# Performance work log

Hardware: AMD Instinct MI355X
Metric: run time of the kernel (lower is better)

The kernel has to match this reference:

```python
import jax, jax.numpy as jnp
import numpy as np

N = 50000
E = 800000
IN_C, HID, OUT_C = 512, 256, 128


def gcn_conv(x, edge_index, W, b, num_nodes):
    # PyG GCNConv: add self-loops, symmetric normalization, linear-then-aggregate.
    h = x @ W  # [N, out]
    src = jnp.concatenate([edge_index[0], jnp.arange(num_nodes)])
    dst = jnp.concatenate([edge_index[1], jnp.arange(num_nodes)])
    ones = jnp.ones(src.shape[0], dtype=x.dtype)
    deg = jax.ops.segment_sum(ones, dst, num_segments=num_nodes)  # in-degree incl. self-loop
    dinv = jax.lax.rsqrt(deg)  # deg >= 1 thanks to self-loops
    norm = dinv[src] * dinv[dst]  # [E+N]
    msg = h[src] * norm[:, None]  # gather + scale
    out = jax.ops.segment_sum(msg, dst, num_segments=num_nodes)  # scatter-add
    return out + b


def setup_inputs() -> dict:
    key = jax.random.key(0)
    k_x, k_e, k_w1, k_b1, k_w2, k_b2 = jax.random.split(key, 6)
    x = jax.random.normal(k_x, (N, IN_C), dtype=jnp.float32)
    edge_index = jax.random.randint(k_e, (2, E), 0, N, dtype=jnp.int64)
    s1 = 1.0 / np.sqrt(IN_C)
    s2 = 1.0 / np.sqrt(HID)
    W1 = jax.random.uniform(k_w1, (IN_C, HID), jnp.float32, -s1, s1)
    b1 = jax.random.uniform(k_b1, (HID,), jnp.float32, -s1, s1)
    W2 = jax.random.uniform(k_w2, (HID, OUT_C), jnp.float32, -s2, s2)
    b2 = jax.random.uniform(k_b2, (OUT_C,), jnp.float32, -s2, s2)
    return {"x": x, "edge_index": edge_index, "W1": W1, "b1": b1, "W2": W2, "b2": b2}


def reference(x, edge_index, W1, b1, W2, b2):
    h = gcn_conv(x, edge_index, W1, b1, N)
    h = jax.nn.relu(h)
    # dropout in eval mode == identity
    return gcn_conv(h, edge_index, W2, b2, N)
```

## Files before the change

### kernel.cpp

```cpp
#include <hip/hip_runtime.h>
#include <stdint.h>

typedef __bf16 bf16_t;
typedef bf16_t bf16x8 __attribute__((ext_vector_type(8)));
typedef bf16_t bf16x4 __attribute__((ext_vector_type(4)));
typedef bf16_t bf16x2 __attribute__((ext_vector_type(2)));
typedef float  f32x4  __attribute__((ext_vector_type(4)));

typedef __attribute__((address_space(3))) void* as3p;
typedef const __attribute__((address_space(1))) void* as1p;

#define IN_C 512
#define HID  256
#define OUTC 128

__global__ void k_prep(const float* __restrict__ W1, const float* __restrict__ W2,
                       const void* __restrict__ ei, int* __restrict__ flag,
                       int* __restrict__ cnt, bf16_t* __restrict__ W1t,
                       bf16_t* __restrict__ W2t, int n) {
  int t = blockIdx.x * blockDim.x + threadIdx.x;
  if (t < IN_C * HID) {
    W1t[(size_t)(t & 255) * IN_C + (t >> 8)] = (bf16_t)W1[t];
    return;
  }
  int u = t - IN_C * HID;
  if (u < HID * OUTC) {
    W2t[(size_t)(u & 127) * HID + (u >> 7)] = (bf16_t)W2[u];
    return;
  }
  u -= HID * OUTC;
  if (u < n) {
    cnt[u] = 0;
    return;
  }
  if (u == n) {
    const long long* p = (const long long*)ei;
    int ok = 1;
    for (int i = 0; i < 64; ++i) {
      long long v = p[i];
      if (v < 0 || v >= n) ok = 0;
    }
    *flag = ok;
  }
}

__global__ void k_hist(const void* __restrict__ ei, const int* __restrict__ flag,
                       int* __restrict__ cnt, int E) {
  int e = blockIdx.x * blockDim.x + threadIdx.x;
  if (e >= E) return;
  int d;
  if (*flag) d = (int)((const long long*)ei)[(size_t)E + e];
  else       d = ((const int*)ei)[E + e];
  atomicAdd(&cnt[d], 1);
}

__global__ void k_scan1(const int* __restrict__ cnt, int* __restrict__ ex,
                        int* __restrict__ part, float* __restrict__ dinv, int n) {
  __shared__ int sh[256];
  int i = blockIdx.x * 256 + threadIdx.x;
  int v = (i < n) ? cnt[i] : 0;
  if (i < n) dinv[i] = rsqrtf((float)v + 1.0f);
  sh[threadIdx.x] = v;
  __syncthreads();
  int val = v;
  for (int off = 1; off < 256; off <<= 1) {
    int t = (threadIdx.x >= off) ? sh[threadIdx.x - off] : 0;
    __syncthreads();
    val += t;
    sh[threadIdx.x] = val;
    __syncthreads();
  }
  if (i < n) ex[i] = val - v;
  if (threadIdx.x == 255) part[blockIdx.x] = val;
}

__global__ void k_scan23(int* __restrict__ rs, const int* __restrict__ part,
                         int* __restrict__ cur, int n, int Etot) {
  __shared__ int sh[256];
  const int b = blockIdx.x, t = threadIdx.x;
  int p = 0;
  for (int j = t; j < b; j += 256) p += part[j];
  sh[t] = p;
  __syncthreads();
  for (int off = 128; off > 0; off >>= 1) {
    if (t < off) sh[t] += sh[t + off];
    __syncthreads();
  }
  int base = sh[0];
  int i = b * 256 + t;
  if (i < n) {
    int r = rs[i] + base;
    rs[i] = r;
    cur[i] = r;
  }
  if (i == 0) rs[n] = Etot;
}

__global__ void k_fill(const void* __restrict__ ei, const int* __restrict__ flag,
                       int* __restrict__ cur, int2* __restrict__ csrw,
                       const float* __restrict__ dinv, int E) {
  int e = blockIdx.x * blockDim.x + threadIdx.x;
  if (e >= E) return;
  int s, d;
  if (*flag) {
    const long long* p = (const long long*)ei;
    s = (int)p[e];
    d = (int)p[(size_t)E + e];
  } else {
    const int* p = (const int*)ei;
    s = p[e];
    d = p[E + e];
  }
  int pos = atomicAdd(&cur[d], 1);
  int2 v;
  v.x = s;
  v.y = __float_as_int(dinv[s]);
  csrw[pos] = v;
}

__global__ __launch_bounds__(512, 2) void k_gemm1(const float* __restrict__ A,
                                                  const bf16_t* __restrict__ Bt,
                                                  bf16_t* __restrict__ C, int n) {
  __shared__ float  As[128 * 32];
  __shared__ bf16_t Bs[256 * 32];
  const int bm = blockIdx.x;
  const int tid = threadIdx.x;
  const int wave = tid >> 6, lane = tid & 63;
  const int wm = (wave >> 2) * 64, wn = (wave & 3) * 64;
  const int quad = lane >> 4, l16 = lane & 15;
  const int rowclamp = n - 1;

  f32x4 acc[4][4];
#pragma unroll
  for (int i = 0; i < 4; ++i)
#pragma unroll
    for (int j = 0; j < 4; ++j)
#pragma unroll
      for (int r = 0; r < 4; ++r) acc[i][j][r] = 0.0f;

  for (int kk = 0; kk < IN_C; kk += 32) {
#pragma unroll
    for (int i = 0; i < 2; ++i) {
      int g = i * 512 + tid;
      int rat = g >> 3, ca = g & 7;
      int garow = bm * 128 + rat;
      if (garow > rowclamp) garow = rowclamp;
      const float* srcA = A + (size_t)garow * IN_C + kk + ((ca ^ (rat & 7)) << 2);
      __builtin_amdgcn_global_load_lds((as1p)srcA,
                                       (as3p)(As + (size_t)(i * 512 + wave * 64) * 4), 16, 0, 0);
      int rbt = g >> 2, cb = g & 3;
      const bf16_t* srcB = Bt + (size_t)rbt * IN_C + kk + ((cb ^ ((rbt >> 1) & 3)) << 3);
      __builtin_amdgcn_global_load_lds((as1p)srcB,
                                       (as3p)(Bs + (size_t)(i * 512 + wave * 64) * 8), 16, 0, 0);
    }
    __syncthreads();
    bf16x8 af[4], bfr[4];
#pragma unroll
    for (int i = 0; i < 4; ++i) {
      int ra = wm + i * 16 + l16;
      const float* base = As + ra * 32;
      int s = ra & 7;
      f32x4 v0 = *(const f32x4*)(base + (((quad * 2) ^ s) << 2));
      f32x4 v1 = *(const f32x4*)(base + (((quad * 2 + 1) ^ s) << 2));
      bf16x8 a;
      a[0] = (bf16_t)v0[0]; a[1] = (bf16_t)v0[1]; a[2] = (bf16_t)v0[2]; a[3] = (bf16_t)v0[3];
      a[4] = (bf16_t)v1[0]; a[5] = (bf16_t)v1[1]; a[6] = (bf16_t)v1[2]; a[7] = (bf16_t)v1[3];
      af[i] = a;
    }
#pragma unroll
    for (int j = 0; j < 4; ++j) {
      int rb = wn + j * 16 + l16;
      bfr[j] = *(const bf16x8*)(Bs + rb * 32 + ((quad ^ ((rb >> 1) & 3)) << 3));
    }
#pragma unroll
    for (int i = 0; i < 4; ++i)
#pragma unroll
      for (int j = 0; j < 4; ++j)
        acc[i][j] = __builtin_amdgcn_mfma_f32_16x16x32_bf16(af[i], bfr[j], acc[i][j], 0, 0, 0);
    __syncthreads();
  }

#pragma unroll
  for (int i = 0; i < 4; ++i) {
#pragma unroll
    for (int j = 0; j < 4; ++j) {
      int col = wn + j * 16 + l16;
      int row0 = bm * 128 + wm + i * 16 + quad * 4;
#pragma unroll
      for (int r = 0; r < 4; ++r)
        C[(size_t)(row0 + r) * HID + col] = (bf16_t)acc[i][j][r];
    }
  }
}

__global__ __launch_bounds__(256, 3) void k_gemm(const bf16_t* __restrict__ A,
                                                 const bf16_t* __restrict__ Bt,
                                                 bf16_t* __restrict__ C,
                                                 int Kdim, int Ncols) {
  __shared__ bf16_t As[128 * 32];
  __shared__ bf16_t Bs[128 * 32];
  const int bm = blockIdx.x, bn = blockIdx.y;
  const int tid = threadIdx.x;
  const int wave = tid >> 6, lane = tid & 63;
  const int wm = (wave >> 1) * 64, wn = (wave & 1) * 64;
  const int quad = lane >> 4, l16 = lane & 15;

  const size_t abase = (size_t)bm * 128 * Kdim;
  const size_t bbase = (size_t)bn * 128 * Kdim;

  f32x4 acc[4][4];
#pragma unroll
  for (int i = 0; i < 4; ++i)
#pragma unroll
    for (int j = 0; j < 4; ++j)
#pragma unroll
      for (int r = 0; r < 4; ++r) acc[i][j][r] = 0.0f;

  for (int kk = 0; kk < Kdim; kk += 32) {
#pragma unroll
    for (int i = 0; i < 2; ++i) {
      int g = i * 256 + tid;
      int row = g >> 2, col = (g & 3) * 8;
      const bf16_t* ga = A + abase + (size_t)row * Kdim + kk + col;
      __builtin_amdgcn_global_load_lds((as1p)ga,
                                       (as3p)(&As[(i * 256 + wave * 64) * 8]), 16, 0, 0);
      const bf16_t* gb = Bt + bbase + (size_t)row * Kdim + kk + col;
      __builtin_amdgcn_global_load_lds((as1p)gb,
                                       (as3p)(&Bs[(i * 256 + wave * 64) * 8]), 16, 0, 0);
    }
    __syncthreads();
    bf16x8 af[4], bf[4];
#pragma unroll
    for (int i = 0; i < 4; ++i)
      af[i] = *(const bf16x8*)(&As[(wm + i * 16 + l16) * 32 + quad * 8]);
#pragma unroll
    for (int j = 0; j < 4; ++j)
      bf[j] = *(const bf16x8*)(&Bs[(wn + j * 16 + l16) * 32 + quad * 8]);
#pragma unroll
    for (int i = 0; i < 4; ++i)
#pragma unroll
      for (int j = 0; j < 4; ++j)
        acc[i][j] = __builtin_amdgcn_mfma_f32_16x16x32_bf16(af[i], bf[j], acc[i][j], 0, 0, 0);
    __syncthreads();
  }

#pragma unroll
  for (int i = 0; i < 4; ++i) {
#pragma unroll
    for (int j = 0; j < 4; ++j) {
      int col = bn * 128 + wn + j * 16 + l16;
      int row0 = bm * 128 + wm + i * 16 + quad * 4;
#pragma unroll
      for (int r = 0; r < 4; ++r)
        C[(size_t)(row0 + r) * Ncols + col] = (bf16_t)acc[i][j][r];
    }
  }
}

__global__ void k_agg_l1(const bf16_t* __restrict__ H, const int* __restrict__ rs,
                         const int2* __restrict__ csrw, const float* __restrict__ dinv,
                         const float* __restrict__ b1, bf16_t* __restrict__ R,
                         int n, int mpad) {
  int d = blockIdx.x * 4 + (threadIdx.x >> 6);
  if (d >= mpad) return;
  int lane = threadIdx.x & 63;
  if (d >= n) {
    bf16x4 z;
    z[0] = (bf16_t)0.0f; z[1] = (bf16_t)0.0f; z[2] = (bf16_t)0.0f; z[3] = (bf16_t)0.0f;
    *(bf16x4*)(R + (size_t)d * HID + lane * 4) = z;
    return;
  }
  int e0 = rs[d], e1 = rs[d + 1];
  float acc[4][4];
  for (int k = 0; k < 4; ++k)
    for (int c = 0; c < 4; ++c) acc[k][c] = 0.f;
  int e = e0;
  for (; e + 8 <= e1; e += 8) {
    int2 cw[8];
    bf16x4 h[8];
#pragma unroll
    for (int u = 0; u < 8; ++u) cw[u] = csrw[e + u];
#pragma unroll
    for (int u = 0; u < 8; ++u)
      h[u] = *(const bf16x4*)(H + (size_t)cw[u].x * HID + lane * 4);
#pragma unroll
    for (int u = 0; u < 8; ++u) {
      float w = __int_as_float(cw[u].y);
#pragma unroll
      for (int c = 0; c < 4; ++c) acc[u & 3][c] += w * (float)h[u][c];
    }
  }
  for (; e < e1; ++e) {
    int2 cw = csrw[e];
    float w = __int_as_float(cw.y);
    bf16x4 hx = *(const bf16x4*)(H + (size_t)cw.x * HID + lane * 4);
#pragma unroll
    for (int c = 0; c < 4; ++c) acc[0][c] += w * (float)hx[c];
  }
  float dd = dinv[d];
  float dv2 = dd * dd;
  bf16x4 hs = *(const bf16x4*)(H + (size_t)d * HID + lane * 4);
  float4 bb = ((const float4*)b1)[lane];
  float a0 = (acc[0][0] + acc[1][0]) + (acc[2][0] + acc[3][0]);
  float a1 = (acc[0][1] + acc[1][1]) + (acc[2][1] + acc[3][1]);
  float a2 = (acc[0][2] + acc[1][2]) + (acc[2][2] + acc[3][2]);
  float a3 = (acc[0][3] + acc[1][3]) + (acc[2][3] + acc[3][3]);
  float v0 = fmaxf(a0 * dd + dv2 * (float)hs[0] + bb.x, 0.f);
  float v1 = fmaxf(a1 * dd + dv2 * (float)hs[1] + bb.y, 0.f);
  float v2 = fmaxf(a2 * dd + dv2 * (float)hs[2] + bb.z, 0.f);
  float v3 = fmaxf(a3 * dd + dv2 * (float)hs[3] + bb.w, 0.f);
  bf16x4 o;
  o[0] = (bf16_t)v0; o[1] = (bf16_t)v1; o[2] = (bf16_t)v2; o[3] = (bf16_t)v3;
  *(bf16x4*)(R + (size_t)d * HID + lane * 4) = o;
}

__global__ void k_agg_l2(const bf16_t* __restrict__ H, const int* __restrict__ rs,
                         const int2* __restrict__ csrw, const float* __restrict__ dinv,
                         const float* __restrict__ b2, float* __restrict__ out, int n) {
  int d = blockIdx.x * 4 + (threadIdx.x >> 6);
  if (d >= n) return;
  int lane = threadIdx.x & 63;
  int e0 = rs[d], e1 = rs[d + 1];
  float acc[4][2];
  for (int k = 0; k < 4; ++k) { acc[k][0] = 0.f; acc[k][1] = 0.f; }
  int e = e0;
  for (; e + 8 <= e1; e += 8) {
    int2 cw[8];
    bf16x2 h[8];
#pragma unroll
    for (int u = 0; u < 8; ++u) cw[u] = csrw[e + u];
#pragma unroll
    for (int u = 0; u < 8; ++u)
      h[u] = *(const bf16x2*)(H + (size_t)cw[u].x * OUTC + lane * 2);
#pragma unroll
    for (int u = 0; u < 8; ++u) {
      float w = __int_as_float(cw[u].y);
      acc[u & 3][0] += w * (float)h[u][0];
      acc[u & 3][1] += w * (float)h[u][1];
    }
  }
  for (; e < e1; ++e) {
    int2 cw = csrw[e];
    float w = __int_as_float(cw.y);
    bf16x2 hx = *(const bf16x2*)(H + (size_t)cw.x * OUTC + lane * 2);
    acc[0][0] += w * (float)hx[0];
    acc[0][1] += w * (float)hx[1];
  }
  float a0 = (acc[0][0] + acc[1][0]) + (acc[2][0] + acc[3][0]);
  float a1 = (acc[0][1] + acc[1][1]) + (acc[2][1] + acc[3][1]);
  float dd = dinv[d];
  float dv2 = dd * dd;
  bf16x2 hs = *(const bf16x2*)(H + (size_t)d * OUTC + lane * 2);
  float2 bb = ((const float2*)b2)[lane];
  float2 o;
  o.x = a0 * dd + dv2 * (float)hs[0] + bb.x;
  o.y = a1 * dd + dv2 * (float)hs[1] + bb.y;
  ((float2*)(out + (size_t)d * OUTC))[lane] = o;
}

extern "C" void kernel_launch(void* const* d_in, const int* in_sizes, int n_in,
                              void* d_out, int out_size, void* d_ws, size_t ws_size,
                              hipStream_t stream) {
  const float* x  = (const float*)d_in[0];
  const void*  ei = d_in[1];
  const float* W1 = (const float*)d_in[2];
  const float* b1 = (const float*)d_in[3];
  const float* W2 = (const float*)d_in[4];
  const float* b2 = (const float*)d_in[5];

  const int n = in_sizes[0] / IN_C;
  const int E = in_sizes[1] / 2;
  const int mpad = (n + 127) & ~127;

  char* w = (char*)d_ws;
  size_t off = 0;
  auto alloc = [&](size_t bytes) -> void* {
    void* p = w + off;
    off = (off + bytes + 255) & ~(size_t)255;
    return p;
  };

  int*    flag = (int*)alloc(4);
  int*    cnt  = (int*)alloc((size_t)n * 4);
  float*  dinv = (float*)alloc((size_t)n * 4);
  int*    rs   = (int*)alloc((size_t)(n + 1) * 4);
  int*    cur  = (int*)alloc((size_t)n * 4);
  int*    part = (int*)alloc(1024);
  int2*   csrw = (int2*)alloc((size_t)E * 8);
  bf16_t* W1t  = (bf16_t*)alloc((size_t)HID * IN_C * 2);
  bf16_t* W2t  = (bf16_t*)alloc((size_t)OUTC * HID * 2);
  bf16_t* H1b  = (bf16_t*)alloc((size_t)mpad * HID * 2);
  bf16_t* R1b  = (bf16_t*)alloc((size_t)mpad * HID * 2);
  bf16_t* H2b  = (bf16_t*)alloc((size_t)mpad * OUTC * 2);
  (void)ws_size; (void)n_in; (void)out_size;

  const int nb = (n + 255) / 256;
  const int prepT = IN_C * HID + HID * OUTC + n + 1;

  k_prep<<<(prepT + 255) / 256, 256, 0, stream>>>(W1, W2, ei, flag, cnt, W1t, W2t, n);
  k_hist<<<(E + 255) / 256, 256, 0, stream>>>(ei, flag, cnt, E);
  k_scan1<<<nb, 256, 0, stream>>>(cnt, rs, part, dinv, n);
  k_scan23<<<nb, 256, 0, stream>>>(rs, part, cur, n, E);
  k_fill<<<(E + 255) / 256, 256, 0, stream>>>(ei, flag, cur, csrw, dinv, E);

  k_gemm1<<<mpad / 128, 512, 0, stream>>>(x, W1t, H1b, n);
  k_agg_l1<<<(mpad + 3) / 4, 256, 0, stream>>>(H1b, rs, csrw, dinv, b1, R1b, n, mpad);
  k_gemm<<<dim3(mpad / 128, 1), 256, 0, stream>>>(R1b, W2t, H2b, HID, OUTC);
  k_agg_l2<<<(n + 3) / 4, 256, 0, stream>>>(H2b, rs, csrw, dinv, b2, (float*)d_out, n);
}
```

Baseline: 379.0 us.

## Widen aggregation gathers to 16-byte loads with multiple edges per wavefront

Both aggregation kernels now have each lane load 8 bf16 features (16 bytes) per neighbor row. Subgroups of the wavefront handle different edges in parallel: two halves in layer 1, four quarters in layer 2. Partial sums are combined with cross-lane shuffles, and the scalar tail loop is replaced by clamped, zero-weighted predicated loads. The aim is fewer, wider memory transactions and more gathers in flight per wave, at the cost of shuffle reductions, wasted work on padded edges, and only a subset of lanes writing results.

```diff
diff --git a/kernel.cpp b/kernel.cpp
--- a/kernel.cpp
+++ b/kernel.cpp
@@ -263,55 +263,60 @@
                          int n, int mpad) {
   int d = blockIdx.x * 4 + (threadIdx.x >> 6);
   if (d >= mpad) return;
-  int lane = threadIdx.x & 63;
+  const int lane = threadIdx.x & 63;
+  const int half = lane >> 5;
+  const int fl = lane & 31;
   if (d >= n) {
-    bf16x4 z;
-    z[0] = (bf16_t)0.0f; z[1] = (bf16_t)0.0f; z[2] = (bf16_t)0.0f; z[3] = (bf16_t)0.0f;
-    *(bf16x4*)(R + (size_t)d * HID + lane * 4) = z;
+    if (lane < 32) {
+      bf16x8 z;
+#pragma unroll
+      for (int j = 0; j < 8; ++j) z[j] = (bf16_t)0.0f;
+      *(bf16x8*)(R + (size_t)d * HID + fl * 8) = z;
+    }
     return;
   }
   int e0 = rs[d], e1 = rs[d + 1];
-  float acc[4][4];
-  for (int k = 0; k < 4; ++k)
-    for (int c = 0; c < 4; ++c) acc[k][c] = 0.f;
-  int e = e0;
-  for (; e + 8 <= e1; e += 8) {
+  float acc0[8], acc1[8];
+#pragma unroll
+  for (int j = 0; j < 8; ++j) { acc0[j] = 0.f; acc1[j] = 0.f; }
+  for (int e = e0; e < e1; e += 16) {
     int2 cw[8];
-    bf16x4 h[8];
-#pragma unroll
-    for (int u = 0; u < 8; ++u) cw[u] = csrw[e + u];
+    float w[8];
+    bf16x8 h[8];
+#pragma unroll
+    for (int u = 0; u < 8; ++u) {
+      int idx = e + 2 * u + half;
+      int ce = idx < e1 ? idx : e1 - 1;
+      cw[u] = csrw[ce];
+      w[u] = idx < e1 ? __int_as_float(cw[u].y) : 0.0f;
+    }
 #pragma unroll
     for (int u = 0; u < 8; ++u)
-      h[u] = *(const bf16x4*)(H + (size_t)cw[u].x * HID + lane * 4);
+      h[u] = *(const bf16x8*)(H + (size_t)cw[u].x * HID + fl * 8);
 #pragma unroll
     for (int u = 0; u < 8; ++u) {
-      float w = __int_as_float(cw[u].y);
-#pragma unroll
-      for (int c = 0; c < 4; ++c) acc[u & 3][c] += w * (float)h[u][c];
-    }
-  }
-  for (; e < e1; ++e) {
-    int2 cw = csrw[e];
-    float w = __int_as_float(cw.y);
-    bf16x4 hx = *(const bf16x4*)(H + (size_t)cw.x * HID + lane * 4);
-#pragma unroll
-    for (int c = 0; c < 4; ++c) acc[0][c] += w * (float)hx[c];
-  }
+      float* A = (u & 1) ? acc1 : acc0;
+#pragma unroll
+      for (int j = 0; j < 8; ++j) A[j] += w[u] * (float)h[u][j];
+    }
+  }
+  float a[8];
+#pragma unroll
+  for (int j = 0; j < 8; ++j) a[j] = acc0[j] + acc1[j];
+#pragma unroll
+  for (int j = 0; j < 8; ++j) a[j] += __shfl_xor(a[j], 32);
   float dd = dinv[d];
   float dv2 = dd * dd;
-  bf16x4 hs = *(const bf16x4*)(H + (size_t)d * HID + lane * 4);
-  float4 bb = ((const float4*)b1)[lane];
-  float a0 = (acc[0][0] + acc[1][0]) + (acc[2][0] + acc[3][0]);
-  float a1 = (acc[0][1] + acc[1][1]) + (acc[2][1] + acc[3][1]);
-  float a2 = (acc[0][2] + acc[1][2]) + (acc[2][2] + acc[3][2]);
-  float a3 = (acc[0][3] + acc[1][3]) + (acc[2][3] + acc[3][3]);
-  float v0 = fmaxf(a0 * dd + dv2 * (float)hs[0] + bb.x, 0.f);
-  float v1 = fmaxf(a1 * dd + dv2 * (float)hs[1] + bb.y, 0.f);
-  float v2 = fmaxf(a2 * dd + dv2 * (float)hs[2] + bb.z, 0.f);
-  float v3 = fmaxf(a3 * dd + dv2 * (float)hs[3] + bb.w, 0.f);
-  bf16x4 o;
-  o[0] = (bf16_t)v0; o[1] = (bf16_t)v1; o[2] = (bf16_t)v2; o[3] = (bf16_t)v3;
-  *(bf16x4*)(R + (size_t)d * HID + lane * 4) = o;
+  bf16x8 hs = *(const bf16x8*)(H + (size_t)d * HID + fl * 8);
+  float4 bb0 = ((const float4*)b1)[fl * 2];
+  float4 bb1 = ((const float4*)b1)[fl * 2 + 1];
+  float bbv[8] = {bb0.x, bb0.y, bb0.z, bb0.w, bb1.x, bb1.y, bb1.z, bb1.w};
+  bf16x8 o;
+#pragma unroll
+  for (int j = 0; j < 8; ++j)
+    o[j] = (bf16_t)fmaxf(a[j] * dd + dv2 * (float)hs[j] + bbv[j], 0.f);
+  if (lane < 32)
+    *(bf16x8*)(R + (size_t)d * HID + fl * 8) = o;
 }
 
 __global__ void k_agg_l2(const bf16_t* __restrict__ H, const int* __restrict__ rs,
@@ -319,43 +324,60 @@
                          const float* __restrict__ b2, float* __restrict__ out, int n) {
   int d = blockIdx.x * 4 + (threadIdx.x >> 6);
   if (d >= n) return;
-  int lane = threadIdx.x & 63;
+  const int lane = threadIdx.x & 63;
+  const int q = (lane >> 4) & 3;
+  const int fl = lane & 15;
   int e0 = rs[d], e1 = rs[d + 1];
-  float acc[4][2];
-  for (int k = 0; k < 4; ++k) { acc[k][0] = 0.f; acc[k][1] = 0.f; }
-  int e = e0;
-  for (; e + 8 <= e1; e += 8) {
+  float acc0[8], acc1[8];
+#pragma unroll
+  for (int j = 0; j < 8; ++j) { acc0[j] = 0.f; acc1[j] = 0.f; }
+  for (int e = e0; e < e1; e += 32) {
     int2 cw[8];
-    bf16x2 h[8];
-#pragma unroll
-    for (int u = 0; u < 8; ++u) cw[u] = csrw[e + u];
+    float w[8];
+    bf16x8 h[8];
+#pragma unroll
+    for (int u = 0; u < 8; ++u) {
+      int idx = e + 4 * u + q;
+      int ce = idx < e1 ? idx : e1 - 1;
+      cw[u] = csrw[ce];
+      w[u] = idx < e1 ? __int_as_float(cw[u].y) : 0.0f;
+    }
 #pragma unroll
     for (int u = 0; u < 8; ++u)
-      h[u] = *(const bf16x2*)(H + (size_t)cw[u].x * OUTC + lane * 2);
+      h[u] = *(const bf16x8*)(H + (size_t)cw[u].x * OUTC + fl * 8);
 #pragma unroll
     for (int u = 0; u < 8; ++u) {
-      float w = __int_as_float(cw[u].y);
-      acc[u & 3][0] += w * (float)h[u][0];
-      acc[u & 3][1] += w * (float)h[u][1];
-    }
-  }
-  for (; e < e1; ++e) {
-    int2 cw = csrw[e];
-    float w = __int_as_float(cw.y);
-    bf16x2 hx = *(const bf16x2*)(H + (size_t)cw.x * OUTC + lane * 2);
-    acc[0][0] += w * (float)hx[0];
-    acc[0][1] += w * (float)hx[1];
-  }
-  float a0 = (acc[0][0] + acc[1][0]) + (acc[2][0] + acc[3][0]);
-  float a1 = (acc[0][1] + acc[1][1]) + (acc[2][1] + acc[3][1]);
+      float* A = (u & 1) ? acc1 : acc0;
+#pragma unroll
+      for (int j = 0; j < 8; ++j) A[j] += w[u] * (float)h[u][j];
+    }
+  }
+  float a[8];
+#pragma unroll
+  for (int j = 0; j < 8; ++j) a[j] = acc0[j] + acc1[j];
+#pragma unroll
+  for (int j = 0; j < 8; ++j) a[j] += __shfl_xor(a[j], 16);
+#pragma unroll
+  for (int j = 0; j < 8; ++j) a[j] += __shfl_xor(a[j], 32);
   float dd = dinv[d];
   float dv2 = dd * dd;
-  bf16x2 hs = *(const bf16x2*)(H + (size_t)d * OUTC + lane * 2);
-  float2 bb = ((const float2*)b2)[lane];
-  float2 o;
-  o.x = a0 * dd + dv2 * (float)hs[0] + bb.x;
-  o.y = a1 * dd + dv2 * (float)hs[1] + bb.y;
-  ((float2*)(out + (size_t)d * OUTC))[lane] = o;
+  bf16x8 hs = *(const bf16x8*)(H + (size_t)d * OUTC + fl * 8);
+  float4 bb0 = ((const float4*)b2)[fl * 2];
+  float4 bb1 = ((const float4*)b2)[fl * 2 + 1];
+  float bbv[8] = {bb0.x, bb0.y, bb0.z, bb0.w, bb1.x, bb1.y, bb1.z, bb1.w};
+  float4 o0, o1;
+  o0.x = a[0] * dd + dv2 * (float)hs[0] + bbv[0];
+  o0.y = a[1] * dd + dv2 * (float)hs[1] + bbv[1];
+  o0.z = a[2] * dd + dv2 * (float)hs[2] + bbv[2];
+  o0.w = a[3] * dd + dv2 * (float)hs[3] + bbv[3];
+  o1.x = a[4] * dd + dv2 * (float)hs[4] + bbv[4];
+  o1.y = a[5] * dd + dv2 * (float)hs[5] + bbv[5];
+  o1.z = a[6] * dd + dv2 * (float)hs[6] + bbv[6];
+  o1.w = a[7] * dd + dv2 * (float)hs[7] + bbv[7];
+  if (lane < 16) {
+    ((float4*)(out + (size_t)d * OUTC))[fl * 2] = o0;
+    ((float4*)(out + (size_t)d * OUTC))[fl * 2 + 1] = o1;
+  }
 }
 
 extern "C" void kernel_launch(void* const* d_in, const int* in_sizes, int n_in,
```

Result: faster. 369.9 us, median of 2 (-2.4%).
